# Optimization experiments

Measured on AMD Instinct MI355X. Metric: run time of the kernel, lower is better.

## Reference

```python
import jax, jax.numpy as jnp
import numpy as np

N_SEGMENT = 16
N_HEADS = 12
DIM = 768
HEAD_DIM = DIM // N_HEADS
LN_EPS = 1e-5


def setup_inputs() -> dict:
    key = jax.random.key(0)
    ks = jax.random.split(key, 12)
    nt, p, c = 512, 197, DIM
    s = 1.0 / np.sqrt(c)
    return {
        "x": jax.random.normal(ks[0], (nt, p, c), dtype=jnp.float32),
        "w1": jax.random.uniform(ks[1], (1, 1, c), dtype=jnp.float32) * 2.0 - 1.0,
        "ln_g": jnp.ones((c,), dtype=jnp.float32),
        "ln_b": jnp.zeros((c,), dtype=jnp.float32),
        "Wq": jax.random.normal(ks[2], (c, c), dtype=jnp.float32) * s,
        "bq": jax.random.normal(ks[3], (c,), dtype=jnp.float32) * 0.02,
        "Wk": jax.random.normal(ks[4], (c, c), dtype=jnp.float32) * s,
        "bk": jax.random.normal(ks[5], (c,), dtype=jnp.float32) * 0.02,
        "Wv": jax.random.normal(ks[6], (c, c), dtype=jnp.float32) * s,
        "bv": jax.random.normal(ks[7], (c,), dtype=jnp.float32) * 0.02,
        "Wo": jax.random.normal(ks[8], (c, c), dtype=jnp.float32) * s,
        "bo": jax.random.normal(ks[9], (c,), dtype=jnp.float32) * 0.02,
    }


def _layer_norm(x, g, b):
    mu = jnp.mean(x, axis=-1, keepdims=True)
    var = jnp.mean(jnp.square(x - mu), axis=-1, keepdims=True)
    return (x - mu) * jax.lax.rsqrt(var + LN_EPS) * g + b


def _attention(h, Wq, bq, Wk, bk, Wv, bv, Wo, bo):
    # h: [B, T, C]
    B, T, C = h.shape
    def heads(y):
        return y.reshape(B, T, N_HEADS, HEAD_DIM).transpose(0, 2, 1, 3)
    q = heads(h @ Wq + bq)  # [B, H, T, Dh]
    k = heads(h @ Wk + bk)
    v = heads(h @ Wv + bv)
    scores = jnp.einsum("bhtd,bhsd->bhts", q, k) / jnp.sqrt(jnp.float32(HEAD_DIM))
    probs = jax.nn.softmax(scores, axis=-1)
    ctx = jnp.einsum("bhts,bhsd->bhtd", probs, v)
    ctx = ctx.transpose(0, 2, 1, 3).reshape(B, T, C)
    return ctx @ Wo + bo


def reference(x, w1, ln_g, ln_b, Wq, bq, Wk, bk, Wv, bv, Wo, bo):
    nt, p, c = x.shape
    B = nt // N_SEGMENT
    xr = x.reshape(B, N_SEGMENT, p, c)
    s = xr[:, :, 0]  # CLS tokens [B, T, C]
    # weighted temporal shift (in torch this mutates the view; residual sees it)
    s_shift = s.at[:, 1:].add(s[:, :-1] * w1)
    t = _layer_norm(s_shift, ln_g, ln_b)
    t = _attention(t, Wq, bq, Wk, bk, Wv, bv, Wo, bo)
    t = t + s_shift  # residual uses SHIFTED tokens (aliasing in torch source)
    out = xr.at[:, :, 0].set(t)
    return out.reshape(nt, p, c)
```

## Files before the change

kernel.cpp:

```cpp
#include <hip/hip_runtime.h>
#include <math.h>

typedef __attribute__((ext_vector_type(8))) short short8;
typedef __attribute__((ext_vector_type(4))) float f32x4;
typedef __attribute__((ext_vector_type(4))) unsigned short us4;

constexpr int NSEG = 16;
constexpr int CC   = 768;
constexpr int PP   = 197;
constexpr int NH   = 12;
constexpr int HD   = 64;
constexpr int NT   = 512;
constexpr int MN   = NT * CC;
constexpr float LN_EPS = 1e-5f;

constexpr unsigned CPT  = 196 * CC / 4;
constexpr unsigned ROW4 = CC / 4;
constexpr unsigned W4TOT = (unsigned)NT * CPT;

constexpr unsigned L1 = 7077888u;
constexpr unsigned L2 = 5406720u;
constexpr unsigned L3 = 4423680u;
constexpr unsigned L4 = W4TOT - L1 - L2 - L3;
constexpr unsigned B2 = L1, B3 = L1 + L2, B4 = L1 + L2 + L3;

__device__ inline unsigned short f2bf(float f) {
    unsigned u = __float_as_uint(f);
    u += 0x7fffu + ((u >> 16) & 1u);
    return (unsigned short)(u >> 16);
}
__device__ inline float bf2f(unsigned short v) {
    return __uint_as_float((unsigned)v << 16);
}
__device__ inline unsigned cidx(unsigned i) {
    unsigned t = i / CPT;
    return i + t * ROW4 + ROW4;
}
__device__ inline void copy_strided(const float* __restrict__ xf, float* __restrict__ of,
                                    unsigned base, unsigned len,
                                    unsigned ct, unsigned nth) {
    const f32x4* __restrict__ x4 = (const f32x4*)xf;
    f32x4* __restrict__ o4 = (f32x4*)of;
    for (unsigned i = ct; i < len; i += nth) {
        unsigned a = cidx(base + i);
        o4[a] = x4[a];
    }
}

template<bool ADD_RES, bool BF16_OUT>
__device__ inline void gemm_tile(const unsigned short* __restrict__ A,
                                 const unsigned short* __restrict__ Bt,
                                 const float* __restrict__ bias,
                                 const float* __restrict__ res,
                                 float* __restrict__ outf, unsigned short* __restrict__ outb,
                                 int by, int bx, size_t orow) {
    int tid  = threadIdx.x;
    int lane = tid & 63, wv = tid >> 6;
    int wr = wv >> 1, wc = wv & 1;
    int l15 = lane & 15, lh = lane >> 4;
    int m0 = by * 64 + wr * 32;
    int n0 = bx * 64 + wc * 32;
    f32x4 acc[2][2] = {};
    const unsigned short* Ar0 = A  + (size_t)(m0 + l15) * CC + lh * 8;
    const unsigned short* Ar1 = Ar0 + 16 * CC;
    const unsigned short* Br0 = Bt + (size_t)(n0 + l15) * CC + lh * 8;
    const unsigned short* Br1 = Br0 + 16 * CC;
    #pragma unroll 4
    for (int k0 = 0; k0 < CC; k0 += 32) {
        short8 a0 = *(const short8*)(Ar0 + k0);
        short8 a1 = *(const short8*)(Ar1 + k0);
        short8 b0 = *(const short8*)(Br0 + k0);
        short8 b1 = *(const short8*)(Br1 + k0);
        acc[0][0] = __builtin_amdgcn_mfma_f32_16x16x32_bf16(a0, b0, acc[0][0], 0, 0, 0);
        acc[0][1] = __builtin_amdgcn_mfma_f32_16x16x32_bf16(a0, b1, acc[0][1], 0, 0, 0);
        acc[1][0] = __builtin_amdgcn_mfma_f32_16x16x32_bf16(a1, b0, acc[1][0], 0, 0, 0);
        acc[1][1] = __builtin_amdgcn_mfma_f32_16x16x32_bf16(a1, b1, acc[1][1], 0, 0, 0);
    }
    #pragma unroll
    for (int mf = 0; mf < 2; ++mf)
        #pragma unroll
        for (int nf = 0; nf < 2; ++nf)
            #pragma unroll
            for (int r = 0; r < 4; ++r) {
                int row = m0 + mf * 16 + lh * 4 + r;
                int col = n0 + nf * 16 + l15;
                float v = acc[mf][nf][r] + bias[col];
                if (ADD_RES) v += res[(size_t)row * CC + col];
                if (BF16_OUT) outb[(size_t)row * orow + col] = f2bf(v);
                else          outf[(size_t)row * orow + col] = v;
            }
}

__global__ __launch_bounds__(256) void k1(const float* __restrict__ x, const float* __restrict__ w1,
        const float* __restrict__ g, const float* __restrict__ bln,
        const float* __restrict__ Wq, const float* __restrict__ Wk,
        const float* __restrict__ Wv, const float* __restrict__ Wo,
        float* __restrict__ s_shift, unsigned short* __restrict__ tln,
        unsigned short* __restrict__ wt, float* __restrict__ out) {
    __shared__ float smem[32 * 33];
    int bid = blockIdx.x, tid = threadIdx.x;
    if (bid < 288) {
        #pragma unroll
        for (int rep = 0; rep < 8; ++rep) {
            int idx = bid + rep * 288;
            int mat = idx / 576, tile = idx % 576;
            int tr = tile / 24, tc = tile % 24;
            const float* W = mat == 0 ? Wq : mat == 1 ? Wk : mat == 2 ? Wv : Wo;
            int lr = tid >> 3, lc = (tid & 7) * 4;
            float4 v = *(const float4*)(W + (size_t)(tr * 32 + lr) * CC + tc * 32 + lc);
            smem[lr * 33 + lc + 0] = v.x; smem[lr * 33 + lc + 1] = v.y;
            smem[lr * 33 + lc + 2] = v.z; smem[lr * 33 + lc + 3] = v.w;
            __syncthreads();
            int ln_ = tid >> 3, kc = (tid & 7) * 4;
            us4 o;
            #pragma unroll
            for (int j = 0; j < 4; ++j) o[j] = f2bf(smem[(kc + j) * 33 + ln_]);
            *(us4*)(wt + (size_t)mat * CC * CC + (size_t)(tc * 32 + ln_) * CC + tr * 32 + kc) = o;
            __syncthreads();
        }
    } else if (bid < 288 + NT) {
        int r = bid - 288, seg = r & (NSEG - 1);
        float vals[3]; float local = 0.f;
        #pragma unroll
        for (int i = 0; i < 3; ++i) {
            int c = tid + i * 256;
            float v = x[(size_t)r * PP * CC + c];
            if (seg > 0) v += w1[c] * x[(size_t)(r - 1) * PP * CC + c];
            vals[i] = v; local += v;
        }
        smem[tid] = local; __syncthreads();
        for (int off = 128; off > 0; off >>= 1) {
            if (tid < off) smem[tid] += smem[tid + off];
            __syncthreads();
        }
        float mu = smem[0] * (1.0f / CC); __syncthreads();
        float lv = 0.f;
        #pragma unroll
        for (int i = 0; i < 3; ++i) { float d = vals[i] - mu; lv += d * d; }
        smem[tid] = lv; __syncthreads();
        for (int off = 128; off > 0; off >>= 1) {
            if (tid < off) smem[tid] += smem[tid + off];
            __syncthreads();
        }
        float rstd = rsqrtf(smem[0] * (1.0f / CC) + LN_EPS);
        #pragma unroll
        for (int i = 0; i < 3; ++i) {
            int c = tid + i * 256;
            s_shift[(size_t)r * CC + c] = vals[i];
            tln[(size_t)r * CC + c] = f2bf((vals[i] - mu) * rstd * g[c] + bln[c]);
        }
    }
    copy_strided(x, out, 0u, L1, (unsigned)bid * 256 + tid, 2048u * 256);
}

__global__ __launch_bounds__(256) void k2(const unsigned short* __restrict__ tln,
        const unsigned short* __restrict__ wt,
        const float* __restrict__ bq, const float* __restrict__ bk, const float* __restrict__ bv,
        unsigned short* __restrict__ qkvb,
        const float* __restrict__ x, float* __restrict__ out) {
    int bid = blockIdx.x, tid = threadIdx.x;
    if (bid < 288) {
        int z = bid / 96, rem = bid % 96;
        int by = rem / 12, bx = rem % 12;
        const float* bias = z == 0 ? bq : (z == 1 ? bk : bv);
        gemm_tile<false, true>(tln, wt + (size_t)z * CC * CC, bias, nullptr,
                               nullptr, qkvb + (size_t)z * MN, by, bx, CC);
    } else {
        copy_strided(x, out, B2, L2, (unsigned)(bid - 288) * 256 + tid, 1760u * 256);
    }
}

__global__ __launch_bounds__(256) void k3(const unsigned short* __restrict__ qkvb,
        unsigned short* __restrict__ ctxb,
        const float* __restrict__ x, float* __restrict__ out) {
    int bid = blockIdx.x, tid = threadIdx.x;
    if (bid < 384) {
        const unsigned short* qb = qkvb;
        const unsigned short* kb = qkvb + MN;
        const unsigned short* vb = qkvb + 2 * MN;
        int bb = bid / NH, h = bid % NH;
        __shared__ float qs[16][HD], ks[16][HD], vs[16][HD];
        __shared__ float sc[16][17];
        __shared__ float rsum[16];
        for (int i = tid; i < 16 * HD; i += 256) {
            int t = i >> 6, d = i & 63;
            size_t gidx = (size_t)(bb * NSEG + t) * CC + h * HD + d;
            qs[t][d] = bf2f(qb[gidx]); ks[t][d] = bf2f(kb[gidx]); vs[t][d] = bf2f(vb[gidx]);
        }
        __syncthreads();
        {
            int t = tid >> 4, s = tid & 15;
            float acc = 0.f;
            #pragma unroll
            for (int d = 0; d < HD; ++d) acc += qs[t][d] * ks[s][d];
            sc[t][s] = acc * 0.125f;
        }
        __syncthreads();
        if (tid < 16) {
            float m = -1e30f;
            #pragma unroll
            for (int s = 0; s < 16; ++s) m = fmaxf(m, sc[tid][s]);
            float sum = 0.f;
            #pragma unroll
            for (int s = 0; s < 16; ++s) { float e = __expf(sc[tid][s] - m); sc[tid][s] = e; sum += e; }
            rsum[tid] = sum;
        }
        __syncthreads();
        for (int i = tid; i < 16 * HD; i += 256) {
            int t = i >> 6, d = i & 63;
            float acc = 0.f;
            #pragma unroll
            for (int s = 0; s < 16; ++s) acc += sc[t][s] * vs[s][d];
            ctxb[(size_t)(bb * NSEG + t) * CC + h * HD + d] = f2bf(acc / rsum[t]);
        }
    } else {
        copy_strided(x, out, B3, L3, (unsigned)(bid - 384) * 256 + tid, 1664u * 256);
    }
}

__global__ __launch_bounds__(256) void k4(const unsigned short* __restrict__ ctxb,
        const unsigned short* __restrict__ wto,
        const float* __restrict__ bo, const float* __restrict__ s_shift,
        float* __restrict__ out, const float* __restrict__ x) {
    int bid = blockIdx.x, tid = threadIdx.x;
    if (bid < 96) {
        int by = bid / 12, bx = bid % 12;
        gemm_tile<true, false>(ctxb, wto, bo, s_shift, out, nullptr, by, bx, (size_t)PP * CC);
    } else {
        copy_strided(x, out, B4, L4, (unsigned)(bid - 96) * 256 + tid, 1952u * 256);
    }
}

extern "C" void kernel_launch(void* const* d_in, const int* in_sizes, int n_in,
                              void* d_out, int out_size, void* d_ws, size_t ws_size,
                              hipStream_t stream) {
    const float* x    = (const float*)d_in[0];
    const float* w1   = (const float*)d_in[1];
    const float* ln_g = (const float*)d_in[2];
    const float* ln_b = (const float*)d_in[3];
    const float* Wq   = (const float*)d_in[4];
    const float* bq   = (const float*)d_in[5];
    const float* Wk   = (const float*)d_in[6];
    const float* bk   = (const float*)d_in[7];
    const float* Wv   = (const float*)d_in[8];
    const float* bv   = (const float*)d_in[9];
    const float* Wo   = (const float*)d_in[10];
    const float* bo   = (const float*)d_in[11];
    float* out = (float*)d_out;

    float* s_shift = (float*)d_ws;
    unsigned short* tln  = (unsigned short*)(s_shift + MN);
    unsigned short* qkvb = tln + MN;
    unsigned short* ctxb = qkvb + 3 * (size_t)MN;
    unsigned short* wt   = ctxb + MN;

    k1<<<2048, 256, 0, stream>>>(x, w1, ln_g, ln_b, Wq, Wk, Wv, Wo, s_shift, tln, wt, out);
    k2<<<2048, 256, 0, stream>>>(tln, wt, bq, bk, bv, qkvb, x, out);
    k3<<<2048, 256, 0, stream>>>(qkvb, ctxb, x, out);
    k4<<<2048, 256, 0, stream>>>(ctxb, wt + (size_t)3 * CC * CC, bo, s_shift, out, x);
}
```

Before: 147.7 us.

## Replace static strided copy with atomic work-stealing chunked copy per kernel

```diff
diff --git a/kernel.cpp b/kernel.cpp
--- a/kernel.cpp
+++ b/kernel.cpp
@@ -18,11 +18,12 @@
 constexpr unsigned ROW4 = CC / 4;
 constexpr unsigned W4TOT = (unsigned)NT * CPT;
 
-constexpr unsigned L1 = 7077888u;
-constexpr unsigned L2 = 5406720u;
-constexpr unsigned L3 = 4423680u;
-constexpr unsigned L4 = W4TOT - L1 - L2 - L3;
-constexpr unsigned B2 = L1, B3 = L1 + L2, B4 = L1 + L2 + L3;
+constexpr unsigned CH4 = 2048;
+constexpr unsigned NCH1 = 215, NCH2 = 165, NCH3 = 135, NCH4 = 73;
+constexpr unsigned S1 = 0;
+constexpr unsigned S2 = S1 + 16u * NCH1 * CH4;
+constexpr unsigned S3 = S2 + 16u * NCH2 * CH4;
+constexpr unsigned S4 = S3 + 16u * NCH3 * CH4;
 
 __device__ inline unsigned short f2bf(float f) {
     unsigned u = __float_as_uint(f);
@@ -36,14 +37,31 @@
     unsigned t = i / CPT;
     return i + t * ROW4 + ROW4;
 }
-__device__ inline void copy_strided(const float* __restrict__ xf, float* __restrict__ of,
-                                    unsigned base, unsigned len,
-                                    unsigned ct, unsigned nth) {
+
+__device__ inline void steal_copy(const float* __restrict__ xf, float* __restrict__ of,
+                                  unsigned* __restrict__ ctrs, unsigned kbase,
+                                  unsigned nchunks) {
+    __shared__ unsigned sc_;
+    int tid = threadIdx.x;
+    unsigned shard = (unsigned)blockIdx.x & 15u;
+    unsigned* c = ctrs + shard * 16u;
+    unsigned base = kbase + shard * nchunks * CH4;
     const f32x4* __restrict__ x4 = (const f32x4*)xf;
     f32x4* __restrict__ o4 = (f32x4*)of;
-    for (unsigned i = ct; i < len; i += nth) {
-        unsigned a = cidx(base + i);
-        o4[a] = x4[a];
+    while (true) {
+        __syncthreads();
+        if (tid == 0) sc_ = atomicAdd(c, 1u);
+        __syncthreads();
+        unsigned ci = sc_;
+        if (ci >= nchunks) break;
+        unsigned start = base + ci * CH4 + tid;
+        unsigned a[8]; f32x4 v[8];
+        #pragma unroll
+        for (int j = 0; j < 8; ++j) a[j] = cidx(start + j * 256);
+        #pragma unroll
+        for (int j = 0; j < 8; ++j) v[j] = x4[a[j]];
+        #pragma unroll
+        for (int j = 0; j < 8; ++j) o4[a[j]] = v[j];
     }
 }
 
@@ -96,7 +114,8 @@
         const float* __restrict__ Wq, const float* __restrict__ Wk,
         const float* __restrict__ Wv, const float* __restrict__ Wo,
         float* __restrict__ s_shift, unsigned short* __restrict__ tln,
-        unsigned short* __restrict__ wt, float* __restrict__ out) {
+        unsigned short* __restrict__ wt, float* __restrict__ out,
+        unsigned* __restrict__ ctrs) {
     __shared__ float smem[32 * 33];
     int bid = blockIdx.x, tid = threadIdx.x;
     if (bid < 288) {
@@ -150,14 +169,15 @@
             tln[(size_t)r * CC + c] = f2bf((vals[i] - mu) * rstd * g[c] + bln[c]);
         }
     }
-    copy_strided(x, out, 0u, L1, (unsigned)bid * 256 + tid, 2048u * 256);
+    steal_copy(x, out, ctrs, S1, NCH1);
 }
 
 __global__ __launch_bounds__(256) void k2(const unsigned short* __restrict__ tln,
         const unsigned short* __restrict__ wt,
         const float* __restrict__ bq, const float* __restrict__ bk, const float* __restrict__ bv,
         unsigned short* __restrict__ qkvb,
-        const float* __restrict__ x, float* __restrict__ out) {
+        const float* __restrict__ x, float* __restrict__ out,
+        unsigned* __restrict__ ctrs) {
     int bid = blockIdx.x, tid = threadIdx.x;
     if (bid < 288) {
         int z = bid / 96, rem = bid % 96;
@@ -165,14 +185,14 @@
         const float* bias = z == 0 ? bq : (z == 1 ? bk : bv);
         gemm_tile<false, true>(tln, wt + (size_t)z * CC * CC, bias, nullptr,
                                nullptr, qkvb + (size_t)z * MN, by, bx, CC);
-    } else {
-        copy_strided(x, out, B2, L2, (unsigned)(bid - 288) * 256 + tid, 1760u * 256);
-    }
+    }
+    steal_copy(x, out, ctrs, S2, NCH2);
 }
 
 __global__ __launch_bounds__(256) void k3(const unsigned short* __restrict__ qkvb,
         unsigned short* __restrict__ ctxb,
-        const float* __restrict__ x, float* __restrict__ out) {
+        const float* __restrict__ x, float* __restrict__ out,
+        unsigned* __restrict__ ctrs) {
     int bid = blockIdx.x, tid = threadIdx.x;
     if (bid < 384) {
         const unsigned short* qb = qkvb;
@@ -213,22 +233,21 @@
             for (int s = 0; s < 16; ++s) acc += sc[t][s] * vs[s][d];
             ctxb[(size_t)(bb * NSEG + t) * CC + h * HD + d] = f2bf(acc / rsum[t]);
         }
-    } else {
-        copy_strided(x, out, B3, L3, (unsigned)(bid - 384) * 256 + tid, 1664u * 256);
-    }
+    }
+    steal_copy(x, out, ctrs, S3, NCH3);
 }
 
 __global__ __launch_bounds__(256) void k4(const unsigned short* __restrict__ ctxb,
         const unsigned short* __restrict__ wto,
         const float* __restrict__ bo, const float* __restrict__ s_shift,
-        float* __restrict__ out, const float* __restrict__ x) {
+        float* __restrict__ out, const float* __restrict__ x,
+        unsigned* __restrict__ ctrs) {
     int bid = blockIdx.x, tid = threadIdx.x;
     if (bid < 96) {
         int by = bid / 12, bx = bid % 12;
         gemm_tile<true, false>(ctxb, wto, bo, s_shift, out, nullptr, by, bx, (size_t)PP * CC);
-    } else {
-        copy_strided(x, out, B4, L4, (unsigned)(bid - 96) * 256 + tid, 1952u * 256);
-    }
+    }
+    steal_copy(x, out, ctrs, S4, NCH4);
 }
 
 extern "C" void kernel_launch(void* const* d_in, const int* in_sizes, int n_in,
@@ -248,14 +267,20 @@
     const float* bo   = (const float*)d_in[11];
     float* out = (float*)d_out;
 
-    float* s_shift = (float*)d_ws;
+    unsigned* ctrs = (unsigned*)d_ws;
+    float* fbase   = (float*)((char*)d_ws + 4096);
+    float* s_shift = fbase;
     unsigned short* tln  = (unsigned short*)(s_shift + MN);
     unsigned short* qkvb = tln + MN;
     unsigned short* ctxb = qkvb + 3 * (size_t)MN;
     unsigned short* wt   = ctxb + MN;
 
-    k1<<<2048, 256, 0, stream>>>(x, w1, ln_g, ln_b, Wq, Wk, Wv, Wo, s_shift, tln, wt, out);
-    k2<<<2048, 256, 0, stream>>>(tln, wt, bq, bk, bv, qkvb, x, out);
-    k3<<<2048, 256, 0, stream>>>(qkvb, ctxb, x, out);
-    k4<<<2048, 256, 0, stream>>>(ctxb, wt + (size_t)3 * CC * CC, bo, s_shift, out, x);
-}
+    (void)hipMemsetAsync(d_ws, 0, 4096, stream);
+
+    k1<<<2048, 256, 0, stream>>>(x, w1, ln_g, ln_b, Wq, Wk, Wv, Wo, s_shift, tln, wt, out,
+                                 ctrs + 0 * 256);
+    k2<<<2048, 256, 0, stream>>>(tln, wt, bq, bk, bv, qkvb, x, out, ctrs + 1 * 256);
+    k3<<<2048, 256, 0, stream>>>(qkvb, ctxb, x, out, ctrs + 2 * 256);
+    k4<<<2048, 256, 0, stream>>>(ctxb, wt + (size_t)3 * CC * CC, bo, s_shift, out, x,
+                                 ctrs + 3 * 256);
+}
```

After: 163.3 us. 1.11x slower.

## Fuse four launches into one persistent kernel with flag-based inter-block dependencies

Applied to the files above, without the earlier changes.

```diff
diff --git a/kernel.cpp b/kernel.cpp
--- a/kernel.cpp
+++ b/kernel.cpp
@@ -17,12 +17,9 @@
 constexpr unsigned CPT  = 196 * CC / 4;
 constexpr unsigned ROW4 = CC / 4;
 constexpr unsigned W4TOT = (unsigned)NT * CPT;
-
-constexpr unsigned L1 = 7077888u;
-constexpr unsigned L2 = 5406720u;
-constexpr unsigned L3 = 4423680u;
-constexpr unsigned L4 = W4TOT - L1 - L2 - L3;
-constexpr unsigned B2 = L1, B3 = L1 + L2, B4 = L1 + L2 + L3;
+constexpr unsigned NBLK = 1024;
+constexpr unsigned GT   = NBLK * 256;
+constexpr unsigned NP   = (W4TOT + GT - 1) / GT;
 
 __device__ inline unsigned short f2bf(float f) {
     unsigned u = __float_as_uint(f);
@@ -36,15 +33,35 @@
     unsigned t = i / CPT;
     return i + t * ROW4 + ROW4;
 }
-__device__ inline void copy_strided(const float* __restrict__ xf, float* __restrict__ of,
-                                    unsigned base, unsigned len,
-                                    unsigned ct, unsigned nth) {
-    const f32x4* __restrict__ x4 = (const f32x4*)xf;
-    f32x4* __restrict__ o4 = (f32x4*)of;
-    for (unsigned i = ct; i < len; i += nth) {
-        unsigned a = cidx(base + i);
-        o4[a] = x4[a];
-    }
+__device__ inline unsigned ldf(unsigned* p) {
+    return __hip_atomic_load(p, __ATOMIC_RELAXED, __HIP_MEMORY_SCOPE_AGENT);
+}
+__device__ inline void signal(unsigned* p, int tid) {
+    __threadfence();
+    __syncthreads();
+    if (tid == 0) __hip_atomic_fetch_add(p, 1u, __ATOMIC_RELEASE, __HIP_MEMORY_SCOPE_AGENT);
+}
+
+__device__ inline void poll_copy(const f32x4* __restrict__ x4, f32x4* __restrict__ o4,
+                                 unsigned g, unsigned* f1, unsigned t1,
+                                 unsigned* f2, unsigned t2, unsigned& curp) {
+    __shared__ unsigned rdy;
+    int tid = threadIdx.x;
+    for (;;) {
+        if (tid == 0) rdy = (ldf(f1) >= t1) && (ldf(f2) >= t2) ? 1u : 0u;
+        __syncthreads();
+        unsigned r = rdy;
+        __syncthreads();
+        if (r) break;
+        if (curp < NP) {
+            unsigned i = curp * GT + g;
+            if (i < W4TOT) { unsigned a = cidx(i); o4[a] = x4[a]; }
+            ++curp;
+        } else {
+            __builtin_amdgcn_s_sleep(8);
+        }
+    }
+    __threadfence();
 }
 
 template<bool ADD_RES, bool BF16_OUT>
@@ -91,19 +108,70 @@
             }
 }
 
-__global__ __launch_bounds__(256) void k1(const float* __restrict__ x, const float* __restrict__ w1,
-        const float* __restrict__ g, const float* __restrict__ bln,
+__global__ __launch_bounds__(256, 4) void mega(
+        const float* __restrict__ x, const float* __restrict__ w1,
+        const float* __restrict__ gg, const float* __restrict__ bln,
         const float* __restrict__ Wq, const float* __restrict__ Wk,
         const float* __restrict__ Wv, const float* __restrict__ Wo,
+        const float* __restrict__ bq, const float* __restrict__ bk,
+        const float* __restrict__ bv, const float* __restrict__ bo,
         float* __restrict__ s_shift, unsigned short* __restrict__ tln,
-        unsigned short* __restrict__ wt, float* __restrict__ out) {
+        unsigned short* __restrict__ qkvb, unsigned short* __restrict__ ctxb,
+        unsigned short* __restrict__ wt, float* __restrict__ out,
+        unsigned* __restrict__ flags) {
     __shared__ float smem[32 * 33];
+    __shared__ float qs[16][HD], ks[16][HD], vs[16][HD];
+    __shared__ float scs[16][17];
+    __shared__ float rsum[16];
+
+    unsigned* ln_f  = flags;
+    unsigned* cvt_f = flags + 16;
+    unsigned* qkv_f = flags + 32;
+    unsigned* att_f = flags + 48;
+
     int bid = blockIdx.x, tid = threadIdx.x;
-    if (bid < 288) {
+    unsigned g = (unsigned)bid * 256 + tid;
+    const f32x4* __restrict__ x4 = (const f32x4*)x;
+    f32x4* __restrict__ o4 = (f32x4*)out;
+
+    if (bid < 512) {
+        int r = bid, seg = r & (NSEG - 1);
+        float vals[3]; float local = 0.f;
+        #pragma unroll
+        for (int i = 0; i < 3; ++i) {
+            int c = tid + i * 256;
+            float v = x[(size_t)r * PP * CC + c];
+            if (seg > 0) v += w1[c] * x[(size_t)(r - 1) * PP * CC + c];
+            vals[i] = v; local += v;
+        }
+        smem[tid] = local; __syncthreads();
+        for (int off = 128; off > 0; off >>= 1) {
+            if (tid < off) smem[tid] += smem[tid + off];
+            __syncthreads();
+        }
+        float mu = smem[0] * (1.0f / CC); __syncthreads();
+        float lv = 0.f;
+        #pragma unroll
+        for (int i = 0; i < 3; ++i) { float d = vals[i] - mu; lv += d * d; }
+        smem[tid] = lv; __syncthreads();
+        for (int off = 128; off > 0; off >>= 1) {
+            if (tid < off) smem[tid] += smem[tid + off];
+            __syncthreads();
+        }
+        float rstd = rsqrtf(smem[0] * (1.0f / CC) + LN_EPS);
+        #pragma unroll
+        for (int i = 0; i < 3; ++i) {
+            int c = tid + i * 256;
+            s_shift[(size_t)r * CC + c] = vals[i];
+            tln[(size_t)r * CC + c] = f2bf((vals[i] - mu) * rstd * gg[c] + bln[c]);
+        }
+        signal(ln_f, tid);
+    } else if (bid < 800) {
+        int idx = bid - 512;
         #pragma unroll
         for (int rep = 0; rep < 8; ++rep) {
-            int idx = bid + rep * 288;
-            int mat = idx / 576, tile = idx % 576;
+            int idx2 = idx + rep * 288;
+            int mat = idx2 / 576, tile = idx2 % 576;
             int tr = tile / 24, tc = tile % 24;
             const float* W = mat == 0 ? Wq : mat == 1 ? Wk : mat == 2 ? Wv : Wo;
             int lr = tid >> 3, lc = (tid & 7) * 4;
@@ -118,70 +186,16 @@
             *(us4*)(wt + (size_t)mat * CC * CC + (size_t)(tc * 32 + ln_) * CC + tr * 32 + kc) = o;
             __syncthreads();
         }
-    } else if (bid < 288 + NT) {
-        int r = bid - 288, seg = r & (NSEG - 1);
-        float vals[3]; float local = 0.f;
-        #pragma unroll
-        for (int i = 0; i < 3; ++i) {
-            int c = tid + i * 256;
-            float v = x[(size_t)r * PP * CC + c];
-            if (seg > 0) v += w1[c] * x[(size_t)(r - 1) * PP * CC + c];
-            vals[i] = v; local += v;
-        }
-        smem[tid] = local; __syncthreads();
-        for (int off = 128; off > 0; off >>= 1) {
-            if (tid < off) smem[tid] += smem[tid + off];
-            __syncthreads();
-        }
-        float mu = smem[0] * (1.0f / CC); __syncthreads();
-        float lv = 0.f;
-        #pragma unroll
-        for (int i = 0; i < 3; ++i) { float d = vals[i] - mu; lv += d * d; }
-        smem[tid] = lv; __syncthreads();
-        for (int off = 128; off > 0; off >>= 1) {
-            if (tid < off) smem[tid] += smem[tid + off];
-            __syncthreads();
-        }
-        float rstd = rsqrtf(smem[0] * (1.0f / CC) + LN_EPS);
-        #pragma unroll
-        for (int i = 0; i < 3; ++i) {
-            int c = tid + i * 256;
-            s_shift[(size_t)r * CC + c] = vals[i];
-            tln[(size_t)r * CC + c] = f2bf((vals[i] - mu) * rstd * g[c] + bln[c]);
-        }
-    }
-    copy_strided(x, out, 0u, L1, (unsigned)bid * 256 + tid, 2048u * 256);
-}
-
-__global__ __launch_bounds__(256) void k2(const unsigned short* __restrict__ tln,
-        const unsigned short* __restrict__ wt,
-        const float* __restrict__ bq, const float* __restrict__ bk, const float* __restrict__ bv,
-        unsigned short* __restrict__ qkvb,
-        const float* __restrict__ x, float* __restrict__ out) {
-    int bid = blockIdx.x, tid = threadIdx.x;
-    if (bid < 288) {
-        int z = bid / 96, rem = bid % 96;
-        int by = rem / 12, bx = rem % 12;
-        const float* bias = z == 0 ? bq : (z == 1 ? bk : bv);
-        gemm_tile<false, true>(tln, wt + (size_t)z * CC * CC, bias, nullptr,
-                               nullptr, qkvb + (size_t)z * MN, by, bx, CC);
-    } else {
-        copy_strided(x, out, B2, L2, (unsigned)(bid - 288) * 256 + tid, 1760u * 256);
-    }
-}
-
-__global__ __launch_bounds__(256) void k3(const unsigned short* __restrict__ qkvb,
-        unsigned short* __restrict__ ctxb,
-        const float* __restrict__ x, float* __restrict__ out) {
-    int bid = blockIdx.x, tid = threadIdx.x;
+        signal(cvt_f, tid);
+    }
+
+    unsigned curp = 0;
     if (bid < 384) {
+        poll_copy(x4, o4, g, qkv_f, 288, qkv_f, 288, curp);
+        int bb = bid / NH, h = bid % NH;
         const unsigned short* qb = qkvb;
         const unsigned short* kb = qkvb + MN;
         const unsigned short* vb = qkvb + 2 * MN;
-        int bb = bid / NH, h = bid % NH;
-        __shared__ float qs[16][HD], ks[16][HD], vs[16][HD];
-        __shared__ float sc[16][17];
-        __shared__ float rsum[16];
         for (int i = tid; i < 16 * HD; i += 256) {
             int t = i >> 6, d = i & 63;
             size_t gidx = (size_t)(bb * NSEG + t) * CC + h * HD + d;
@@ -193,16 +207,16 @@
             float acc = 0.f;
             #pragma unroll
             for (int d = 0; d < HD; ++d) acc += qs[t][d] * ks[s][d];
-            sc[t][s] = acc * 0.125f;
+            scs[t][s] = acc * 0.125f;
         }
         __syncthreads();
         if (tid < 16) {
             float m = -1e30f;
             #pragma unroll
-            for (int s = 0; s < 16; ++s) m = fmaxf(m, sc[tid][s]);
+            for (int s = 0; s < 16; ++s) m = fmaxf(m, scs[tid][s]);
             float sum = 0.f;
             #pragma unroll
-            for (int s = 0; s < 16; ++s) { float e = __expf(sc[tid][s] - m); sc[tid][s] = e; sum += e; }
+            for (int s = 0; s < 16; ++s) { float e = __expf(scs[tid][s] - m); scs[tid][s] = e; sum += e; }
             rsum[tid] = sum;
         }
         __syncthreads();
@@ -210,24 +224,28 @@
             int t = i >> 6, d = i & 63;
             float acc = 0.f;
             #pragma unroll
-            for (int s = 0; s < 16; ++s) acc += sc[t][s] * vs[s][d];
+            for (int s = 0; s < 16; ++s) acc += scs[t][s] * vs[s][d];
             ctxb[(size_t)(bb * NSEG + t) * CC + h * HD + d] = f2bf(acc / rsum[t]);
         }
-    } else {
-        copy_strided(x, out, B3, L3, (unsigned)(bid - 384) * 256 + tid, 1664u * 256);
-    }
-}
-
-__global__ __launch_bounds__(256) void k4(const unsigned short* __restrict__ ctxb,
-        const unsigned short* __restrict__ wto,
-        const float* __restrict__ bo, const float* __restrict__ s_shift,
-        float* __restrict__ out, const float* __restrict__ x) {
-    int bid = blockIdx.x, tid = threadIdx.x;
-    if (bid < 96) {
-        int by = bid / 12, bx = bid % 12;
-        gemm_tile<true, false>(ctxb, wto, bo, s_shift, out, nullptr, by, bx, (size_t)PP * CC);
-    } else {
-        copy_strided(x, out, B4, L4, (unsigned)(bid - 96) * 256 + tid, 1952u * 256);
+        signal(att_f, tid);
+    } else if (bid < 480) {
+        poll_copy(x4, o4, g, att_f, 384, att_f, 384, curp);
+        int j = bid - 384;
+        gemm_tile<true, false>(ctxb, wt + (size_t)3 * CC * CC, bo, s_shift,
+                               out, nullptr, j / 12, j % 12, (size_t)PP * CC);
+    } else if (bid >= 512 && bid < 800) {
+        poll_copy(x4, o4, g, ln_f, 512, cvt_f, 288, curp);
+        int idx = bid - 512;
+        int z = idx / 96, rem = idx % 96;
+        const float* bias = z == 0 ? bq : (z == 1 ? bk : bv);
+        gemm_tile<false, true>(tln, wt + (size_t)z * CC * CC, bias, nullptr,
+                               nullptr, qkvb + (size_t)z * MN, rem / 12, rem % 12, CC);
+        signal(qkv_f, tid);
+    }
+
+    for (; curp < NP; ++curp) {
+        unsigned i = curp * GT + g;
+        if (i < W4TOT) { unsigned a = cidx(i); o4[a] = x4[a]; }
     }
 }
 
@@ -248,14 +266,17 @@
     const float* bo   = (const float*)d_in[11];
     float* out = (float*)d_out;
 
-    float* s_shift = (float*)d_ws;
+    unsigned* flags = (unsigned*)d_ws;
+    float* fbase   = (float*)((char*)d_ws + 4096);
+    float* s_shift = fbase;
     unsigned short* tln  = (unsigned short*)(s_shift + MN);
     unsigned short* qkvb = tln + MN;
     unsigned short* ctxb = qkvb + 3 * (size_t)MN;
     unsigned short* wt   = ctxb + MN;
 
-    k1<<<2048, 256, 0, stream>>>(x, w1, ln_g, ln_b, Wq, Wk, Wv, Wo, s_shift, tln, wt, out);
-    k2<<<2048, 256, 0, stream>>>(tln, wt, bq, bk, bv, qkvb, x, out);
-    k3<<<2048, 256, 0, stream>>>(qkvb, ctxb, x, out);
-    k4<<<2048, 256, 0, stream>>>(ctxb, wt + (size_t)3 * CC * CC, bo, s_shift, out, x);
-}
+    (void)hipMemsetAsync(d_ws, 0, 256, stream);
+
+    mega<<<NBLK, 256, 0, stream>>>(x, w1, ln_g, ln_b, Wq, Wk, Wv, Wo,
+                                   bq, bk, bv, bo,
+                                   s_shift, tln, qkvb, ctxb, wt, out, flags);
+}
```

After: 575.7 us. +289.9%, slower.

## Replace overlapped strided copy with a single device memcpy before compute kernels

Applied to the files above, without the earlier changes.

```diff
diff --git a/kernel.cpp b/kernel.cpp
--- a/kernel.cpp
+++ b/kernel.cpp
@@ -14,16 +14,6 @@
 constexpr int MN   = NT * CC;
 constexpr float LN_EPS = 1e-5f;
 
-constexpr unsigned CPT  = 196 * CC / 4;
-constexpr unsigned ROW4 = CC / 4;
-constexpr unsigned W4TOT = (unsigned)NT * CPT;
-
-constexpr unsigned L1 = 7077888u;
-constexpr unsigned L2 = 5406720u;
-constexpr unsigned L3 = 4423680u;
-constexpr unsigned L4 = W4TOT - L1 - L2 - L3;
-constexpr unsigned B2 = L1, B3 = L1 + L2, B4 = L1 + L2 + L3;
-
 __device__ inline unsigned short f2bf(float f) {
     unsigned u = __float_as_uint(f);
     u += 0x7fffu + ((u >> 16) & 1u);
@@ -31,20 +21,6 @@
 }
 __device__ inline float bf2f(unsigned short v) {
     return __uint_as_float((unsigned)v << 16);
-}
-__device__ inline unsigned cidx(unsigned i) {
-    unsigned t = i / CPT;
-    return i + t * ROW4 + ROW4;
-}
-__device__ inline void copy_strided(const float* __restrict__ xf, float* __restrict__ of,
-                                    unsigned base, unsigned len,
-                                    unsigned ct, unsigned nth) {
-    const f32x4* __restrict__ x4 = (const f32x4*)xf;
-    f32x4* __restrict__ o4 = (f32x4*)of;
-    for (unsigned i = ct; i < len; i += nth) {
-        unsigned a = cidx(base + i);
-        o4[a] = x4[a];
-    }
 }
 
 template<bool ADD_RES, bool BF16_OUT>
@@ -96,7 +72,7 @@
         const float* __restrict__ Wq, const float* __restrict__ Wk,
         const float* __restrict__ Wv, const float* __restrict__ Wo,
         float* __restrict__ s_shift, unsigned short* __restrict__ tln,
-        unsigned short* __restrict__ wt, float* __restrict__ out) {
+        unsigned short* __restrict__ wt) {
     __shared__ float smem[32 * 33];
     int bid = blockIdx.x, tid = threadIdx.x;
     if (bid < 288) {
@@ -118,7 +94,7 @@
             *(us4*)(wt + (size_t)mat * CC * CC + (size_t)(tc * 32 + ln_) * CC + tr * 32 + kc) = o;
             __syncthreads();
         }
-    } else if (bid < 288 + NT) {
+    } else {
         int r = bid - 288, seg = r & (NSEG - 1);
         float vals[3]; float local = 0.f;
         #pragma unroll
@@ -150,85 +126,70 @@
             tln[(size_t)r * CC + c] = f2bf((vals[i] - mu) * rstd * g[c] + bln[c]);
         }
     }
-    copy_strided(x, out, 0u, L1, (unsigned)bid * 256 + tid, 2048u * 256);
 }
 
 __global__ __launch_bounds__(256) void k2(const unsigned short* __restrict__ tln,
         const unsigned short* __restrict__ wt,
         const float* __restrict__ bq, const float* __restrict__ bk, const float* __restrict__ bv,
-        unsigned short* __restrict__ qkvb,
-        const float* __restrict__ x, float* __restrict__ out) {
+        unsigned short* __restrict__ qkvb) {
+    int bid = blockIdx.x;
+    int z = bid / 96, rem = bid % 96;
+    int by = rem / 12, bx = rem % 12;
+    const float* bias = z == 0 ? bq : (z == 1 ? bk : bv);
+    gemm_tile<false, true>(tln, wt + (size_t)z * CC * CC, bias, nullptr,
+                           nullptr, qkvb + (size_t)z * MN, by, bx, CC);
+}
+
+__global__ __launch_bounds__(256) void k3(const unsigned short* __restrict__ qkvb,
+        unsigned short* __restrict__ ctxb) {
     int bid = blockIdx.x, tid = threadIdx.x;
-    if (bid < 288) {
-        int z = bid / 96, rem = bid % 96;
-        int by = rem / 12, bx = rem % 12;
-        const float* bias = z == 0 ? bq : (z == 1 ? bk : bv);
-        gemm_tile<false, true>(tln, wt + (size_t)z * CC * CC, bias, nullptr,
-                               nullptr, qkvb + (size_t)z * MN, by, bx, CC);
-    } else {
-        copy_strided(x, out, B2, L2, (unsigned)(bid - 288) * 256 + tid, 1760u * 256);
-    }
-}
-
-__global__ __launch_bounds__(256) void k3(const unsigned short* __restrict__ qkvb,
-        unsigned short* __restrict__ ctxb,
-        const float* __restrict__ x, float* __restrict__ out) {
-    int bid = blockIdx.x, tid = threadIdx.x;
-    if (bid < 384) {
-        const unsigned short* qb = qkvb;
-        const unsigned short* kb = qkvb + MN;
-        const unsigned short* vb = qkvb + 2 * MN;
-        int bb = bid / NH, h = bid % NH;
-        __shared__ float qs[16][HD], ks[16][HD], vs[16][HD];
-        __shared__ float sc[16][17];
-        __shared__ float rsum[16];
-        for (int i = tid; i < 16 * HD; i += 256) {
-            int t = i >> 6, d = i & 63;
-            size_t gidx = (size_t)(bb * NSEG + t) * CC + h * HD + d;
-            qs[t][d] = bf2f(qb[gidx]); ks[t][d] = bf2f(kb[gidx]); vs[t][d] = bf2f(vb[gidx]);
-        }
-        __syncthreads();
-        {
-            int t = tid >> 4, s = tid & 15;
-            float acc = 0.f;
-            #pragma unroll
-            for (int d = 0; d < HD; ++d) acc += qs[t][d] * ks[s][d];
-            sc[t][s] = acc * 0.125f;
-        }
-        __syncthreads();
-        if (tid < 16) {
-            float m = -1e30f;
-            #pragma unroll
-            for (int s = 0; s < 16; ++s) m = fmaxf(m, sc[tid][s]);
-            float sum = 0.f;
-            #pragma unroll
-            for (int s = 0; s < 16; ++s) { float e = __expf(sc[tid][s] - m); sc[tid][s] = e; sum += e; }
-            rsum[tid] = sum;
-        }
-        __syncthreads();
-        for (int i = tid; i < 16 * HD; i += 256) {
-            int t = i >> 6, d = i & 63;
-            float acc = 0.f;
-            #pragma unroll
-            for (int s = 0; s < 16; ++s) acc += sc[t][s] * vs[s][d];
-            ctxb[(size_t)(bb * NSEG + t) * CC + h * HD + d] = f2bf(acc / rsum[t]);
-        }
-    } else {
-        copy_strided(x, out, B3, L3, (unsigned)(bid - 384) * 256 + tid, 1664u * 256);
+    const unsigned short* qb = qkvb;
+    const unsigned short* kb = qkvb + MN;
+    const unsigned short* vb = qkvb + 2 * MN;
+    int bb = bid / NH, h = bid % NH;
+    __shared__ float qs[16][HD], ks[16][HD], vs[16][HD];
+    __shared__ float sc[16][17];
+    __shared__ float rsum[16];
+    for (int i = tid; i < 16 * HD; i += 256) {
+        int t = i >> 6, d = i & 63;
+        size_t gidx = (size_t)(bb * NSEG + t) * CC + h * HD + d;
+        qs[t][d] = bf2f(qb[gidx]); ks[t][d] = bf2f(kb[gidx]); vs[t][d] = bf2f(vb[gidx]);
+    }
+    __syncthreads();
+    {
+        int t = tid >> 4, s = tid & 15;
+        float acc = 0.f;
+        #pragma unroll
+        for (int d = 0; d < HD; ++d) acc += qs[t][d] * ks[s][d];
+        sc[t][s] = acc * 0.125f;
+    }
+    __syncthreads();
+    if (tid < 16) {
+        float m = -1e30f;
+        #pragma unroll
+        for (int s = 0; s < 16; ++s) m = fmaxf(m, sc[tid][s]);
+        float sum = 0.f;
+        #pragma unroll
+        for (int s = 0; s < 16; ++s) { float e = __expf(sc[tid][s] - m); sc[tid][s] = e; sum += e; }
+        rsum[tid] = sum;
+    }
+    __syncthreads();
+    for (int i = tid; i < 16 * HD; i += 256) {
+        int t = i >> 6, d = i & 63;
+        float acc = 0.f;
+        #pragma unroll
+        for (int s = 0; s < 16; ++s) acc += sc[t][s] * vs[s][d];
+        ctxb[(size_t)(bb * NSEG + t) * CC + h * HD + d] = f2bf(acc / rsum[t]);
     }
 }
 
 __global__ __launch_bounds__(256) void k4(const unsigned short* __restrict__ ctxb,
         const unsigned short* __restrict__ wto,
         const float* __restrict__ bo, const float* __restrict__ s_shift,
-        float* __restrict__ out, const float* __restrict__ x) {
-    int bid = blockIdx.x, tid = threadIdx.x;
-    if (bid < 96) {
-        int by = bid / 12, bx = bid % 12;
-        gemm_tile<true, false>(ctxb, wto, bo, s_shift, out, nullptr, by, bx, (size_t)PP * CC);
-    } else {
-        copy_strided(x, out, B4, L4, (unsigned)(bid - 96) * 256 + tid, 1952u * 256);
-    }
+        float* __restrict__ out) {
+    int bid = blockIdx.x;
+    int by = bid / 12, bx = bid % 12;
+    gemm_tile<true, false>(ctxb, wto, bo, s_shift, out, nullptr, by, bx, (size_t)PP * CC);
 }
 
 extern "C" void kernel_launch(void* const* d_in, const int* in_sizes, int n_in,
@@ -254,8 +215,10 @@
     unsigned short* ctxb = qkvb + 3 * (size_t)MN;
     unsigned short* wt   = ctxb + MN;
 
-    k1<<<2048, 256, 0, stream>>>(x, w1, ln_g, ln_b, Wq, Wk, Wv, Wo, s_shift, tln, wt, out);
-    k2<<<2048, 256, 0, stream>>>(tln, wt, bq, bk, bv, qkvb, x, out);
-    k3<<<2048, 256, 0, stream>>>(qkvb, ctxb, x, out);
-    k4<<<2048, 256, 0, stream>>>(ctxb, wt + (size_t)3 * CC * CC, bo, s_shift, out, x);
-}
+    k1<<<800, 256, 0, stream>>>(x, w1, ln_g, ln_b, Wq, Wk, Wv, Wo, s_shift, tln, wt);
+    (void)hipMemcpyAsync(out, x, (size_t)NT * PP * CC * sizeof(float),
+                         hipMemcpyDeviceToDevice, stream);
+    k2<<<288, 256, 0, stream>>>(tln, wt, bq, bk, bv, qkvb);
+    k3<<<384, 256, 0, stream>>>(qkvb, ctxb);
+    k4<<<96, 256, 0, stream>>>(ctxb, wt + (size_t)3 * CC * CC, bo, s_shift, out);
+}
```

Result: slower. 194.6 us (+31.8%).
